# Kernel optimization log

Measured on AMD Instinct MI355X. Metric: run time of the kernel, lower is better.

## Reference

```python
import jax, jax.numpy as jnp
import numpy as np

B, S, D = 2, 1024, 768
E = 8
FF = 4 * D
TOP_K = 2
LN_EPS = 1e-5


def setup_inputs() -> dict:
    key = jax.random.key(0)
    ks = jax.random.split(key, 14)
    s = 0.02
    return {
        "x": jax.random.normal(ks[0], (B, S, D), dtype=jnp.float32),
        "router_w": jax.random.normal(ks[1], (D, E), dtype=jnp.float32) * s,
        "router_b": jnp.zeros((E,), dtype=jnp.float32),
        "dg_w": jax.random.normal(ks[2], (E, D), dtype=jnp.float32) * s,
        "dg_b": jnp.zeros((E,), dtype=jnp.float32),
        "w1_w": jax.random.normal(ks[3], (E, D, FF), dtype=jnp.float32) * s,
        "w1_b": jnp.zeros((E, FF), dtype=jnp.float32),
        "w2_w": jax.random.normal(ks[4], (E, FF, D), dtype=jnp.float32) * s,
        "w2_b": jnp.zeros((E, D), dtype=jnp.float32),
        "w3_w": jax.random.normal(ks[5], (E, D, FF), dtype=jnp.float32) * s,
        "w3_b": jnp.zeros((E, FF), dtype=jnp.float32),
        "ln_g": jnp.ones((E, D), dtype=jnp.float32),
        "ln_b": jnp.zeros((E, D), dtype=jnp.float32),
    }


def _moe_forward(x, router_w, router_b, dg_w, dg_b, w1_w, w1_b, w2_w, w2_b,
                 w3_w, w3_b, ln_g, ln_b):
    b, s, d = x.shape
    T = b * s
    xf = x.reshape(T, d)

    # Router (dropout is identity in eval mode)
    logits = xf @ router_w + router_b                      # [T, E]
    routing = jax.nn.softmax(logits, axis=-1)
    topk_w, topk_i = jax.lax.top_k(routing, TOP_K)          # [T, 2]
    topk_w = jax.nn.softmax(topk_w, axis=-1)                # renormalize via softmax (as in source)

    # Dense per-expert SwiGLU FFN over all tokens (faithful math, vectorized)
    h1 = jnp.einsum('td,edf->etf', xf, w1_w) + w1_b[:, None, :]   # [E, T, FF]
    gate = jax.nn.silu(jnp.einsum('td,edf->etf', xf, w3_w) + w3_b[:, None, :])
    ff = jnp.einsum('etf,efd->etd', jax.nn.silu(h1) * gate, w2_w) + w2_b[:, None, :]  # [E, T, D]
    dg = jax.nn.sigmoid(jnp.einsum('td,ed->et', xf, dg_w) + dg_b[:, None])            # [E, T]

    tok = jnp.arange(T)
    out = jnp.zeros_like(xf)
    for i in range(TOP_K):
        e = topk_i[:, i]                                    # [T]
        y = xf + dg[e, tok][:, None] * topk_w[:, i:i + 1] * ff[e, tok]  # [T, D]
        mu = jnp.mean(y, axis=-1, keepdims=True)
        var = jnp.mean(jnp.square(y - mu), axis=-1, keepdims=True)
        out = out + ((y - mu) / jnp.sqrt(var + LN_EPS)) * ln_g[e] + ln_b[e]

    expert_load = jnp.zeros((E,), dtype=jnp.float32).at[topk_i.reshape(-1)].add(1.0)
    return out.reshape(b, s, d), expert_load


def reference(x, router_w, router_b, dg_w, dg_b, w1_w, w1_b, w2_w, w2_b,
              w3_w, w3_b, ln_g, ln_b):
    return _moe_forward(x, router_w, router_b, dg_w, dg_b, w1_w, w1_b,
                        w2_w, w2_b, w3_w, w3_b, ln_g, ln_b)
```

## Files before the change

### kernel.cpp

```cpp
#include <hip/hip_runtime.h>
#include <math.h>

#define T 2048
#define D 768
#define E 8
#define FF 3072
#define NPOS (2 * T)
#define MAXTILE 40
#define PSTRIDE ((size_t)(NPOS + 128) * D)

using f32x4 = __attribute__((ext_vector_type(4))) float;

template<bool HI>
__device__ __forceinline__ unsigned f2fp8pk(float a, float b, unsigned old) {
    return __builtin_amdgcn_cvt_pk_fp8_f32(a, b, (int)old, HI);
}
__device__ __forceinline__ unsigned char f2fp8(float f) {
    return (unsigned char)(__builtin_amdgcn_cvt_pk_fp8_f32(f, 0.f, 0, false) & 0xff);
}
__device__ __forceinline__ float siluf(float v) {
    return v / (1.0f + __expf(-v));
}
__device__ __forceinline__ void gload16(const void* g, void* l) {
    __builtin_amdgcn_global_load_lds(
        (const __attribute__((address_space(1))) void*)g,
        (__attribute__((address_space(3))) void*)l, 16, 0, 0);
}

__device__ __forceinline__ void transpose128(const float* __restrict__ in,
                                             unsigned char* __restrict__ out,
                                             int C, int Rb, int r0, int c0,
                                             char* smem, int tid) {
    int wv = tid >> 6, lane = tid & 63;
    size_t rowB = (size_t)C * 4;
    const char* inb = (const char*)in + (size_t)r0 * rowB + (size_t)c0 * 4;
    const char* src_lane = inb + (size_t)(lane >> 5) * rowB + (lane & 31) * 16;
#pragma unroll
    for (int i = 0; i < 16; ++i) {
        int rpair = i * 4 + wv;
        gload16(src_lane + (size_t)(2 * rpair) * rowB, smem + rpair * 1024);
    }
    asm volatile("s_waitcnt vmcnt(0)" ::: "memory");
    __syncthreads();

    const float* fin = (const float*)smem;
    int cb = (tid & 31) * 4;
    int rgb = tid >> 5;
    unsigned pk[4][4];
#pragma unroll
    for (int p = 0; p < 4; ++p) {
        int rb = (rgb + 8 * p) * 4;
        float4 q0 = *(const float4*)(fin + (rb + 0) * 128 + cb);
        float4 q1 = *(const float4*)(fin + (rb + 1) * 128 + cb);
        float4 q2 = *(const float4*)(fin + (rb + 2) * 128 + cb);
        float4 q3 = *(const float4*)(fin + (rb + 3) * 128 + cb);
        unsigned w;
        w = f2fp8pk<false>(q0.x, q1.x, 0); w = f2fp8pk<true>(q2.x, q3.x, w); pk[p][0] = w;
        w = f2fp8pk<false>(q0.y, q1.y, 0); w = f2fp8pk<true>(q2.y, q3.y, w); pk[p][1] = w;
        w = f2fp8pk<false>(q0.z, q1.z, 0); w = f2fp8pk<true>(q2.z, q3.z, w); pk[p][2] = w;
        w = f2fp8pk<false>(q0.w, q1.w, 0); w = f2fp8pk<true>(q2.w, q3.w, w); pk[p][3] = w;
    }
    __syncthreads();
    unsigned* po = (unsigned*)smem;
#pragma unroll
    for (int p = 0; p < 4; ++p) {
        int rg = rgb + 8 * p;
#pragma unroll
        for (int j = 0; j < 4; ++j)
            po[(cb + j) * 33 + rg] = pk[p][j];
    }
    __syncthreads();
#pragma unroll
    for (int p = 0; p < 4; ++p) {
        int c = (tid >> 3) + 32 * p;
        int gs = tid & 7;
        const unsigned* bp = &po[c * 33 + gs * 4];
        uint4 val;
        val.x = bp[0]; val.y = bp[1]; val.z = bp[2]; val.w = bp[3];
        *(uint4*)(out + (size_t)(c0 + c) * Rb + r0 + gs * 16) = val;
    }
}

__global__ __launch_bounds__(256, 2)
void pre_kernel(const float* __restrict__ x,
                const float* __restrict__ rw, const float* __restrict__ rbias,
                const float* __restrict__ dgw, const float* __restrict__ dgb,
                const float* __restrict__ w1, const float* __restrict__ w3,
                unsigned char* __restrict__ xb,
                int* __restrict__ e_arr, float* __restrict__ s_arr,
                unsigned char* __restrict__ w1t, unsigned char* __restrict__ w3t) {
    __shared__ __align__(16) char smem[65536];
    int bid = blockIdx.x;
    int tid = threadIdx.x;

    if (bid >= 512) {
        int idx = bid - 512;
        int z = idx / 144;
        int rem = idx % 144;
        int r0 = (rem % 6) * 128;
        int c0 = (rem / 6) * 128;
        const float* in;
        unsigned char* outp;
        if (z < 8) { in = w1 + (size_t)z * D * FF; outp = w1t + (size_t)z * D * FF; }
        else       { in = w3 + (size_t)(z - 8) * D * FF; outp = w3t + (size_t)(z - 8) * D * FF; }
        transpose128(in, outp, FF, D, r0, c0, smem, tid);
        return;
    }

    int lane = tid & 63;
    int wv = tid >> 6;
    int t = bid * 4 + wv;

    float lg[E], dl[E];
#pragma unroll
    for (int e = 0; e < E; ++e) { lg[e] = 0.f; dl[e] = 0.f; }

    const float* xt = x + (size_t)t * D;
    unsigned char* xbt = xb + (size_t)t * D;
#pragma unroll
    for (int i = 0; i < D / 64; ++i) {
        int d = lane + 64 * i;
        float xv = xt[d];
        xbt[d] = f2fp8(xv);
#pragma unroll
        for (int e = 0; e < E; ++e) {
            lg[e] = fmaf(xv, rw[d * E + e], lg[e]);
            dl[e] = fmaf(xv, dgw[e * D + d], dl[e]);
        }
    }
#pragma unroll
    for (int e = 0; e < E; ++e) {
        for (int off = 32; off; off >>= 1) {
            lg[e] += __shfl_xor(lg[e], off);
            dl[e] += __shfl_xor(dl[e], off);
        }
    }
    if (lane == 0) {
        float p[E];
        float m = -1e30f;
#pragma unroll
        for (int e = 0; e < E; ++e) { lg[e] += rbias[e]; m = fmaxf(m, lg[e]); }
        float s = 0.f;
#pragma unroll
        for (int e = 0; e < E; ++e) { p[e] = __expf(lg[e] - m); s += p[e]; }
        float inv = 1.0f / s;
#pragma unroll
        for (int e = 0; e < E; ++e) p[e] *= inv;

        int i0 = 0; float b0 = p[0];
#pragma unroll
        for (int e = 1; e < E; ++e) if (p[e] > b0) { b0 = p[e]; i0 = e; }
        int i1 = -1; float b1 = -1.0f;
#pragma unroll
        for (int e = 0; e < E; ++e) if (e != i0 && p[e] > b1) { b1 = p[e]; i1 = e; }

        float eb = __expf(b1 - b0);
        float w0 = 1.0f / (1.0f + eb);
        float w1v = eb / (1.0f + eb);

        float dg0 = 1.0f / (1.0f + __expf(-(dl[i0] + dgb[i0])));
        float dg1 = 1.0f / (1.0f + __expf(-(dl[i1] + dgb[i1])));

        e_arr[t * 2 + 0] = i0;
        e_arr[t * 2 + 1] = i1;
        s_arr[t * 2 + 0] = dg0 * w0;
        s_arr[t * 2 + 1] = dg1 * w1v;
    }
}

__global__ __launch_bounds__(256)
void scan_assign_kernel(const int* __restrict__ e_arr,
                        float* __restrict__ load_out,
                        int* __restrict__ tme, int* __restrict__ tmm,
                        int* __restrict__ tml,
                        int* __restrict__ a_tok,
                        int* __restrict__ pos_of) {
    __shared__ int lcnt[E];
    __shared__ int lcur[E];
    int tid = threadIdx.x;
    if (tid < E) lcnt[tid] = 0;
    __syncthreads();
    for (int t = tid; t < T; t += 256) {
        atomicAdd(&lcnt[e_arr[t * 2]], 1);
        atomicAdd(&lcnt[e_arr[t * 2 + 1]], 1);
    }
    __syncthreads();
    if (tid == 0) {
        int b = 0, nt = 0;
        for (int e = 0; e < E; ++e) {
            int c = lcnt[e];
            lcur[e] = b;
            load_out[e] = (float)c;
            for (int m = 0; m < c; m += 128) {
                tme[nt] = e;
                tmm[nt] = b + m;
                tml[nt] = (c - m < 128) ? (c - m) : 128;
                ++nt;
            }
            b += c;
        }
        for (; nt < MAXTILE; ++nt) tme[nt] = -1;
    }
    __syncthreads();
    for (int t = tid; t < T; t += 256) {
#pragma unroll
        for (int s = 0; s < 2; ++s) {
            int e = e_arr[t * 2 + s];
            int pos = atomicAdd(&lcur[e], 1);
            a_tok[pos] = t;
            pos_of[t * 2 + s] = pos;
        }
    }
}

__global__ __launch_bounds__(256, 2)
void gemm1_w2t_kernel(const float* __restrict__ w2, unsigned char* __restrict__ w2t,
                      const unsigned char* __restrict__ xb,
                      const unsigned char* __restrict__ w1t, const float* __restrict__ w1b,
                      const unsigned char* __restrict__ w3t, const float* __restrict__ w3b,
                      const int* __restrict__ a_tok,
                      const int* __restrict__ tme, const int* __restrict__ tmm,
                      const int* __restrict__ tml,
                      unsigned char* __restrict__ acts) {
    __shared__ __align__(16) char smem[65536];
    int bid = blockIdx.x;
    int tid = threadIdx.x;

    if (bid < 1152) {
        int z = bid / 144;
        int rem = bid % 144;
        int r0 = (rem % 24) * 128;
        int c0 = (rem / 24) * 128;
        transpose128(w2 + (size_t)z * FF * D, w2t + (size_t)z * FF * D,
                     D, FF, r0, c0, smem, tid);
        return;
    }

    int g = bid - 1152;
    int mt = g / 48;
    int e = tme[mt];
    if (e < 0) return;
    int mstart = tmm[mt], mlen = tml[mt];
    int fBase = (g % 48) * 64;

    char (*As)[16384] = (char(*)[16384])smem;
    char (*Bs)[16384] = (char(*)[16384])(smem + 32768);

    int lane = tid & 63, wv = tid >> 6;
    int wr = wv & 1, wc = wv >> 1;
    int l15 = lane & 15, lk = lane >> 4;
    int lrow = lane >> 3;
    int swl = (((lane & 7) ^ lrow) << 4);

    const char* xbp = (const char*)xb;
    size_t aoff[4];
#pragma unroll
    for (int i = 0; i < 4; ++i) {
        int r = (wv + 4 * i) * 8 + lrow;
        int rr = r < mlen ? r : mlen - 1;
        aoff[i] = (size_t)a_tok[mstart + rr] * D + swl;
    }
    const char* w1p = (const char*)(w1t + (size_t)e * FF * D);
    const char* w3p = (const char*)(w3t + (size_t)e * FF * D);
    size_t boff[2];
#pragma unroll
    for (int i = 0; i < 2; ++i) {
        int f = (wv + 4 * i) * 8 + lrow;
        boff[i] = (size_t)(fBase + f) * D + swl;
    }

    auto stage = [&](int buf, int ks) {
        int kb = ks * 128;
        char* ab = &As[buf][0];
        char* bb = &Bs[buf][0];
#pragma unroll
        for (int i = 0; i < 4; ++i)
            gload16(xbp + aoff[i] + kb, ab + (wv + 4 * i) * 1024);
#pragma unroll
        for (int i = 0; i < 2; ++i) {
            gload16(w1p + boff[i] + kb, bb + (wv + 4 * i) * 1024);
            gload16(w3p + boff[i] + kb, bb + 8192 + (wv + 4 * i) * 1024);
        }
    };

    f32x4 hacc[4][2], gacc[4][2];
#pragma unroll
    for (int m = 0; m < 4; ++m)
#pragma unroll
        for (int n = 0; n < 2; ++n) {
            hacc[m][n] = f32x4{0.f, 0.f, 0.f, 0.f};
            gacc[m][n] = f32x4{0.f, 0.f, 0.f, 0.f};
        }

    stage(0, 0);
    stage(1, 1);
#pragma unroll 1
    for (int ks = 0; ks < 6; ++ks) {
        int cur = ks & 1;
        if (ks < 5) asm volatile("s_waitcnt vmcnt(8)" ::: "memory");
        else        asm volatile("s_waitcnt vmcnt(0)" ::: "memory");
        __builtin_amdgcn_s_barrier();
        const char* Ab = &As[cur][0];
        const char* Bb = &Bs[cur][0];
        __builtin_amdgcn_s_setprio(1);
#pragma unroll
        for (int ksub = 0; ksub < 4; ++ksub) {
            int koff = ksub * 32 + lk * 8;
            long af[4];
#pragma unroll
            for (int m = 0; m < 4; ++m) {
                int row = wr * 64 + m * 16 + l15;
                af[m] = *(const long*)(Ab + row * 128 + (koff ^ ((row & 7) << 4)));
            }
#pragma unroll
            for (int n = 0; n < 2; ++n) {
                int rowf = wc * 32 + n * 16 + l15;
                int off = rowf * 128 + (koff ^ ((rowf & 7) << 4));
                long b1 = *(const long*)(Bb + off);
                long b3 = *(const long*)(Bb + 8192 + off);
#pragma unroll
                for (int m = 0; m < 4; ++m) {
                    hacc[m][n] = __builtin_amdgcn_mfma_f32_16x16x32_fp8_fp8(af[m], b1, hacc[m][n], 0, 0, 0);
                    gacc[m][n] = __builtin_amdgcn_mfma_f32_16x16x32_fp8_fp8(af[m], b3, gacc[m][n], 0, 0, 0);
                }
            }
        }
        __builtin_amdgcn_s_setprio(0);
        __builtin_amdgcn_s_barrier();
        if (ks < 4) stage(cur, ks + 2);
    }

    unsigned char* al = (unsigned char*)&As[0][0];
    float b1v[2], b3v[2];
#pragma unroll
    for (int n = 0; n < 2; ++n) {
        int f = fBase + wc * 32 + n * 16 + l15;
        b1v[n] = w1b[e * FF + f];
        b3v[n] = w3b[e * FF + f];
    }
#pragma unroll
    for (int m = 0; m < 4; ++m)
#pragma unroll
        for (int n = 0; n < 2; ++n)
#pragma unroll
            for (int j = 0; j < 4; ++j) {
                float h = hacc[m][n][j] + b1v[n];
                float gg = gacc[m][n][j] + b3v[n];
                int row = wr * 64 + m * 16 + lk * 4 + j;
                int col = wc * 32 + n * 16 + l15;
                al[row * 64 + col] = f2fp8(siluf(h) * siluf(gg));
            }
    __syncthreads();
    int r = tid >> 1, cb = (tid & 1) * 32;
    if (r < mlen) {
        unsigned char* gp = acts + (size_t)(mstart + r) * FF + fBase + cb;
        const unsigned char* lp = al + r * 64 + cb;
        *(uint4*)(gp)      = *(const uint4*)(lp);
        *(uint4*)(gp + 16) = *(const uint4*)(lp + 16);
    }
}

__global__ __launch_bounds__(256, 2)
void gemm2_kernel(const unsigned char* __restrict__ acts,
                  const unsigned char* __restrict__ w2t,
                  const int* __restrict__ tme, const int* __restrict__ tmm,
                  const int* __restrict__ tml,
                  float* __restrict__ ffs) {
    int mt = blockIdx.y;
    int e = tme[mt];
    if (e < 0) return;
    int mstart = tmm[mt], mlen = tml[mt];
    int nBase = blockIdx.x * 128;
    int ksl = blockIdx.z;

    __shared__ char As[2][16384];
    __shared__ char Bs[2][16384];

    int tid = threadIdx.x;
    int lane = tid & 63, wv = tid >> 6;
    int wr = wv & 1, wc = wv >> 1;
    int l15 = lane & 15, lk = lane >> 4;
    int lrow = lane >> 3;
    int swl = (((lane & 7) ^ lrow) << 4);

    const char* ap = (const char*)acts;
    const char* w2p = (const char*)(w2t + (size_t)e * (size_t)D * FF);
    size_t aoff[4], boff[4];
#pragma unroll
    for (int i = 0; i < 4; ++i) {
        int r = (wv + 4 * i) * 8 + lrow;
        aoff[i] = (size_t)(mstart + r) * FF + swl;
        boff[i] = (size_t)(nBase + r) * FF + swl;
    }
    int kOff = ksl * (FF / 2);

    auto stage = [&](int buf, int ks) {
        int kb = kOff + ks * 128;
        char* ab = &As[buf][0];
        char* bb = &Bs[buf][0];
#pragma unroll
        for (int i = 0; i < 4; ++i) {
            gload16(ap + aoff[i] + kb, ab + (wv + 4 * i) * 1024);
            gload16(w2p + boff[i] + kb, bb + (wv + 4 * i) * 1024);
        }
    };

    f32x4 facc[4][4];
#pragma unroll
    for (int m = 0; m < 4; ++m)
#pragma unroll
        for (int n = 0; n < 4; ++n) facc[m][n] = f32x4{0.f, 0.f, 0.f, 0.f};

    stage(0, 0);
    stage(1, 1);
#pragma unroll 1
    for (int ks = 0; ks < 12; ++ks) {
        int cur = ks & 1;
        if (ks < 11) asm volatile("s_waitcnt vmcnt(8)" ::: "memory");
        else         asm volatile("s_waitcnt vmcnt(0)" ::: "memory");
        __builtin_amdgcn_s_barrier();
        const char* Ab = &As[cur][0];
        const char* Bb = &Bs[cur][0];
        __builtin_amdgcn_s_setprio(1);
#pragma unroll
        for (int ksub = 0; ksub < 4; ++ksub) {
            int koff = ksub * 32 + lk * 8;
            long af[4], bf[4];
#pragma unroll
            for (int m = 0; m < 4; ++m) {
                int row = wr * 64 + m * 16 + l15;
                af[m] = *(const long*)(Ab + row * 128 + (koff ^ ((row & 7) << 4)));
            }
#pragma unroll
            for (int n = 0; n < 4; ++n) {
                int row = wc * 64 + n * 16 + l15;
                bf[n] = *(const long*)(Bb + row * 128 + (koff ^ ((row & 7) << 4)));
            }
#pragma unroll
            for (int m = 0; m < 4; ++m)
#pragma unroll
                for (int n = 0; n < 4; ++n)
                    facc[m][n] = __builtin_amdgcn_mfma_f32_16x16x32_fp8_fp8(af[m], bf[n], facc[m][n], 0, 0, 0);
        }
        __builtin_amdgcn_s_setprio(0);
        __builtin_amdgcn_s_barrier();
        if (ks < 10) stage(cur, ks + 2);
    }

    float* op = ffs + (size_t)ksl * PSTRIDE;
#pragma unroll
    for (int m = 0; m < 4; ++m)
#pragma unroll
        for (int j = 0; j < 4; ++j) {
            int row = wr * 64 + m * 16 + lk * 4 + j;
            if (row < mlen) {
                float* gp = op + (size_t)(mstart + row) * D + nBase + wc * 64;
#pragma unroll
                for (int n = 0; n < 4; ++n)
                    gp[n * 16 + l15] = facc[m][n][j];
            }
        }
}

__global__ __launch_bounds__(256)
void combine_kernel(const float* __restrict__ x,
                    const float* __restrict__ ffs,
                    const int* __restrict__ e_arr,
                    const int* __restrict__ pos_of,
                    const float* __restrict__ s_arr,
                    const float* __restrict__ w2b,
                    const float* __restrict__ lng,
                    const float* __restrict__ lnb,
                    float* __restrict__ out) {
    int t = blockIdx.x;
    int tid = threadIdx.x;
    int p0 = pos_of[t * 2], p1 = pos_of[t * 2 + 1];
    int e0 = e_arr[t * 2], e1 = e_arr[t * 2 + 1];
    float sw0 = s_arr[t * 2], sw1 = s_arr[t * 2 + 1];
    __shared__ float red[4][4];

    float y0[3], y1[3];
    float s0 = 0.f, q0 = 0.f, s1 = 0.f, q1 = 0.f;
#pragma unroll
    for (int m = 0; m < 3; ++m) {
        int d = tid + 256 * m;
        float xv = x[(size_t)t * D + d];
        float f0 = ffs[(size_t)p0 * D + d] + ffs[PSTRIDE + (size_t)p0 * D + d] + w2b[e0 * D + d];
        float f1 = ffs[(size_t)p1 * D + d] + ffs[PSTRIDE + (size_t)p1 * D + d] + w2b[e1 * D + d];
        float a = xv + sw0 * f0;
        float bb = xv + sw1 * f1;
        y0[m] = a; y1[m] = bb;
        s0 += a; q0 += a * a;
        s1 += bb; q1 += bb * bb;
    }
    for (int off = 32; off; off >>= 1) {
        s0 += __shfl_xor(s0, off);
        q0 += __shfl_xor(q0, off);
        s1 += __shfl_xor(s1, off);
        q1 += __shfl_xor(q1, off);
    }
    int wv = tid >> 6, lane = tid & 63;
    if (lane == 0) { red[wv][0] = s0; red[wv][1] = q0; red[wv][2] = s1; red[wv][3] = q1; }
    __syncthreads();
    s0 = red[0][0] + red[1][0] + red[2][0] + red[3][0];
    q0 = red[0][1] + red[1][1] + red[2][1] + red[3][1];
    s1 = red[0][2] + red[1][2] + red[2][2] + red[3][2];
    q1 = red[0][3] + red[1][3] + red[2][3] + red[3][3];

    const float invD = 1.0f / (float)D;
    float mu0 = s0 * invD, var0 = q0 * invD - mu0 * mu0;
    float mu1 = s1 * invD, var1 = q1 * invD - mu1 * mu1;
    float r0 = rsqrtf(var0 + 1e-5f);
    float r1 = rsqrtf(var1 + 1e-5f);

#pragma unroll
    for (int m = 0; m < 3; ++m) {
        int d = tid + 256 * m;
        out[(size_t)t * D + d] =
            (y0[m] - mu0) * r0 * lng[e0 * D + d] + lnb[e0 * D + d] +
            (y1[m] - mu1) * r1 * lng[e1 * D + d] + lnb[e1 * D + d];
    }
}

extern "C" void kernel_launch(void* const* d_in, const int* in_sizes, int n_in,
                              void* d_out, int out_size, void* d_ws, size_t ws_size,
                              hipStream_t stream) {
    const float* x   = (const float*)d_in[0];
    const float* rw  = (const float*)d_in[1];
    const float* rb  = (const float*)d_in[2];
    const float* dgw = (const float*)d_in[3];
    const float* dgb = (const float*)d_in[4];
    const float* w1  = (const float*)d_in[5];
    const float* w1b = (const float*)d_in[6];
    const float* w2  = (const float*)d_in[7];
    const float* w2b = (const float*)d_in[8];
    const float* w3  = (const float*)d_in[9];
    const float* w3b = (const float*)d_in[10];
    const float* lng = (const float*)d_in[11];
    const float* lnb = (const float*)d_in[12];

    float* out = (float*)d_out;
    float* load_out = out + (size_t)T * D;

    char* w = (char*)d_ws;
    size_t off = 0;
    auto alloc = [&](size_t bytes) -> void* {
        void* p = w + off;
        off = (off + bytes + 255) & ~(size_t)255;
        return p;
    };
    int* e_arr    = (int*)alloc(NPOS * sizeof(int));
    int* a_tok    = (int*)alloc(NPOS * sizeof(int));
    int* pos_of   = (int*)alloc(NPOS * sizeof(int));
    float* s_arr  = (float*)alloc(NPOS * sizeof(float));
    int* tme      = (int*)alloc(MAXTILE * sizeof(int));
    int* tmm      = (int*)alloc(MAXTILE * sizeof(int));
    int* tml      = (int*)alloc(MAXTILE * sizeof(int));
    unsigned char* xb  = (unsigned char*)alloc((size_t)T * D);
    unsigned char* w1t = (unsigned char*)alloc((size_t)E * D * FF);
    unsigned char* w3t = (unsigned char*)alloc((size_t)E * D * FF);
    unsigned char* w2t = (unsigned char*)alloc((size_t)E * D * FF);
    unsigned char* acts = (unsigned char*)alloc((size_t)(NPOS + 128) * FF);
    float* ffs    = (float*)alloc(2 * PSTRIDE * sizeof(float));

    pre_kernel<<<512 + 2304, 256, 0, stream>>>(x, rw, rb, dgw, dgb, w1, w3,
                                               xb, e_arr, s_arr, w1t, w3t);
    scan_assign_kernel<<<1, 256, 0, stream>>>(e_arr, load_out, tme, tmm, tml,
                                              a_tok, pos_of);
    gemm1_w2t_kernel<<<1152 + 1920, 256, 0, stream>>>(
        w2, w2t, xb, w1t, w1b, w3t, w3b, a_tok, tme, tmm, tml, acts);
    gemm2_kernel<<<dim3(D / 128, MAXTILE, 2), 256, 0, stream>>>(
        acts, w2t, tme, tmm, tml, ffs);
    combine_kernel<<<T, 256, 0, stream>>>(x, ffs, e_arr, pos_of, s_arr, w2b, lng, lnb, out);
}
```

Before: 153.4 us.

## Process two M-tiles per gemm1 block with cross-tile prefetch pipelining

Measured after the change: 148.3 us. 3.3% less time.

```diff
diff --git a/kernel.cpp b/kernel.cpp
--- a/kernel.cpp
+++ b/kernel.cpp
@@ -222,13 +222,14 @@
                       const int* __restrict__ tme, const int* __restrict__ tmm,
                       const int* __restrict__ tml,
                       unsigned char* __restrict__ acts) {
-    __shared__ __align__(16) char smem[65536];
+    __shared__ __align__(16) char smem[73728];
     int bid = blockIdx.x;
     int tid = threadIdx.x;
 
-    if (bid < 1152) {
-        int z = bid / 144;
-        int rem = bid % 144;
+    if (bid >= 960) {
+        int idx = bid - 960;
+        int z = idx / 144;
+        int rem = idx % 144;
         int r0 = (rem % 24) * 128;
         int c0 = (rem / 24) * 128;
         transpose128(w2 + (size_t)z * FF * D, w2t + (size_t)z * FF * D,
@@ -236,15 +237,21 @@
         return;
     }
 
-    int g = bid - 1152;
-    int mt = g / 48;
-    int e = tme[mt];
-    if (e < 0) return;
-    int mstart = tmm[mt], mlen = tml[mt];
-    int fBase = (g % 48) * 64;
-
-    char (*As)[16384] = (char(*)[16384])smem;
-    char (*Bs)[16384] = (char(*)[16384])(smem + 32768);
+    int slot = bid / 48;
+    int fBase = (bid % 48) * 64;
+    int mt0 = slot * 2;
+    int e0 = tme[mt0];
+    if (e0 < 0) return;
+    int e1 = tme[mt0 + 1];
+    bool have2 = (e1 >= 0);
+    int mstart0 = tmm[mt0], mlen0 = tml[mt0];
+    int mstart1 = have2 ? tmm[mt0 + 1] : mstart0;
+    int mlen1   = have2 ? tml[mt0 + 1] : mlen0;
+    if (!have2) e1 = e0;
+
+    char* As = smem;
+    char* Bs = smem + 32768;
+    unsigned char* eplds = (unsigned char*)(smem + 65536);
 
     int lane = tid & 63, wv = tid >> 6;
     int wr = wv & 1, wc = wv >> 1;
@@ -253,15 +260,11 @@
     int swl = (((lane & 7) ^ lrow) << 4);
 
     const char* xbp = (const char*)xb;
-    size_t aoff[4];
-#pragma unroll
-    for (int i = 0; i < 4; ++i) {
-        int r = (wv + 4 * i) * 8 + lrow;
-        int rr = r < mlen ? r : mlen - 1;
-        aoff[i] = (size_t)a_tok[mstart + rr] * D + swl;
-    }
-    const char* w1p = (const char*)(w1t + (size_t)e * FF * D);
-    const char* w3p = (const char*)(w3t + (size_t)e * FF * D);
+    const char* w1p0 = (const char*)(w1t + (size_t)e0 * FF * D);
+    const char* w3p0 = (const char*)(w3t + (size_t)e0 * FF * D);
+    const char* w1p1 = (const char*)(w1t + (size_t)e1 * FF * D);
+    const char* w3p1 = (const char*)(w3t + (size_t)e1 * FF * D);
+
     size_t boff[2];
 #pragma unroll
     for (int i = 0; i < 2; ++i) {
@@ -269,39 +272,53 @@
         boff[i] = (size_t)(fBase + f) * D + swl;
     }
 
-    auto stage = [&](int buf, int ks) {
+    size_t a0[4], a1[4];
+#pragma unroll
+    for (int i = 0; i < 4; ++i) {
+        int r = (wv + 4 * i) * 8 + lrow;
+        int rr0 = r < mlen0 ? r : mlen0 - 1;
+        int rr1 = r < mlen1 ? r : mlen1 - 1;
+        a0[i] = (size_t)a_tok[mstart0 + rr0] * D + swl;
+        a1[i] = (size_t)a_tok[mstart1 + rr1] * D + swl;
+    }
+    float tb1[2][2], tb3[2][2];
+#pragma unroll
+    for (int n = 0; n < 2; ++n) {
+        int f = fBase + wc * 32 + n * 16 + l15;
+        tb1[0][n] = w1b[e0 * FF + f];
+        tb3[0][n] = w3b[e0 * FF + f];
+        tb1[1][n] = w1b[e1 * FF + f];
+        tb3[1][n] = w3b[e1 * FF + f];
+    }
+
+    auto stage = [&](int buf, const size_t* ao, const char* w1p_, const char* w3p_, int ks) {
         int kb = ks * 128;
-        char* ab = &As[buf][0];
-        char* bb = &Bs[buf][0];
+        char* ab = As + buf * 16384;
+        char* bb = Bs + buf * 16384;
 #pragma unroll
         for (int i = 0; i < 4; ++i)
-            gload16(xbp + aoff[i] + kb, ab + (wv + 4 * i) * 1024);
+            gload16(xbp + ao[i] + kb, ab + (wv + 4 * i) * 1024);
 #pragma unroll
         for (int i = 0; i < 2; ++i) {
-            gload16(w1p + boff[i] + kb, bb + (wv + 4 * i) * 1024);
-            gload16(w3p + boff[i] + kb, bb + 8192 + (wv + 4 * i) * 1024);
+            gload16(w1p_ + boff[i] + kb, bb + (wv + 4 * i) * 1024);
+            gload16(w3p_ + boff[i] + kb, bb + 8192 + (wv + 4 * i) * 1024);
         }
     };
 
     f32x4 hacc[4][2], gacc[4][2];
-#pragma unroll
-    for (int m = 0; m < 4; ++m)
-#pragma unroll
-        for (int n = 0; n < 2; ++n) {
-            hacc[m][n] = f32x4{0.f, 0.f, 0.f, 0.f};
-            gacc[m][n] = f32x4{0.f, 0.f, 0.f, 0.f};
-        }
-
-    stage(0, 0);
-    stage(1, 1);
-#pragma unroll 1
-    for (int ks = 0; ks < 6; ++ks) {
-        int cur = ks & 1;
-        if (ks < 5) asm volatile("s_waitcnt vmcnt(8)" ::: "memory");
-        else        asm volatile("s_waitcnt vmcnt(0)" ::: "memory");
-        __builtin_amdgcn_s_barrier();
-        const char* Ab = &As[cur][0];
-        const char* Bb = &Bs[cur][0];
+    auto zacc = [&]() {
+#pragma unroll
+        for (int m = 0; m < 4; ++m)
+#pragma unroll
+            for (int n = 0; n < 2; ++n) {
+                hacc[m][n] = f32x4{0.f, 0.f, 0.f, 0.f};
+                gacc[m][n] = f32x4{0.f, 0.f, 0.f, 0.f};
+            }
+    };
+
+    auto computeStep = [&](int buf) {
+        const char* Ab = As + buf * 16384;
+        const char* Bb = Bs + buf * 16384;
         __builtin_amdgcn_s_setprio(1);
 #pragma unroll
         for (int ksub = 0; ksub < 4; ++ksub) {
@@ -326,38 +343,63 @@
             }
         }
         __builtin_amdgcn_s_setprio(0);
-        __builtin_amdgcn_s_barrier();
-        if (ks < 4) stage(cur, ks + 2);
-    }
-
-    unsigned char* al = (unsigned char*)&As[0][0];
-    float b1v[2], b3v[2];
-#pragma unroll
-    for (int n = 0; n < 2; ++n) {
-        int f = fBase + wc * 32 + n * 16 + l15;
-        b1v[n] = w1b[e * FF + f];
-        b3v[n] = w3b[e * FF + f];
-    }
-#pragma unroll
-    for (int m = 0; m < 4; ++m)
-#pragma unroll
-        for (int n = 0; n < 2; ++n)
-#pragma unroll
-            for (int j = 0; j < 4; ++j) {
-                float h = hacc[m][n][j] + b1v[n];
-                float gg = gacc[m][n][j] + b3v[n];
-                int row = wr * 64 + m * 16 + lk * 4 + j;
-                int col = wc * 32 + n * 16 + l15;
-                al[row * 64 + col] = f2fp8(siluf(h) * siluf(gg));
-            }
-    __syncthreads();
-    int r = tid >> 1, cb = (tid & 1) * 32;
-    if (r < mlen) {
-        unsigned char* gp = acts + (size_t)(mstart + r) * FF + fBase + cb;
-        const unsigned char* lp = al + r * 64 + cb;
-        *(uint4*)(gp)      = *(const uint4*)(lp);
-        *(uint4*)(gp + 16) = *(const uint4*)(lp + 16);
-    }
+    };
+
+    auto epilogueT = [&](const float b1v[2], const float b3v[2], int mstart_, int mlen_) {
+#pragma unroll
+        for (int m = 0; m < 4; ++m)
+#pragma unroll
+            for (int n = 0; n < 2; ++n)
+#pragma unroll
+                for (int j = 0; j < 4; ++j) {
+                    float h = hacc[m][n][j] + b1v[n];
+                    float gg = gacc[m][n][j] + b3v[n];
+                    int row = wr * 64 + m * 16 + lk * 4 + j;
+                    int col = wc * 32 + n * 16 + l15;
+                    eplds[row * 64 + col] = f2fp8(siluf(h) * siluf(gg));
+                }
+        __syncthreads();
+        int r = tid >> 1, cb = (tid & 1) * 32;
+        if (r < mlen_) {
+            unsigned char* gp = acts + (size_t)(mstart_ + r) * FF + fBase + cb;
+            const unsigned char* lp = eplds + r * 64 + cb;
+            *(uint4*)(gp)      = *(const uint4*)(lp);
+            *(uint4*)(gp + 16) = *(const uint4*)(lp + 16);
+        }
+    };
+
+#define G1_WAIT8 asm volatile("s_waitcnt vmcnt(8)" ::: "memory")
+#define G1_BAR   __builtin_amdgcn_s_barrier()
+
+    zacc();
+    stage(0, a0, w1p0, w3p0, 0);
+    stage(1, a0, w1p0, w3p0, 1);
+    asm volatile("s_waitcnt vmcnt(0)" ::: "memory");
+    __syncthreads();
+
+     computeStep(0); G1_BAR; stage(0, a0, w1p0, w3p0, 2);
+     G1_BAR; computeStep(1); G1_BAR; stage(1, a0, w1p0, w3p0, 3);
+     G1_WAIT8; G1_BAR; computeStep(0); G1_BAR; stage(0, a0, w1p0, w3p0, 4);
+     G1_WAIT8; G1_BAR; computeStep(1); G1_BAR; stage(1, a0, w1p0, w3p0, 5);
+     G1_WAIT8; G1_BAR; computeStep(0); G1_BAR; stage(0, a1, w1p1, w3p1, 0);
+     G1_WAIT8; G1_BAR; computeStep(1); G1_BAR; stage(1, a1, w1p1, w3p1, 1);
+
+    epilogueT(tb1[0], tb3[0], mstart0, mlen0);
+    asm volatile("s_waitcnt vmcnt(0)" ::: "memory");
+    __syncthreads();
+
+    if (have2) {
+        zacc();
+         computeStep(0); G1_BAR; stage(0, a1, w1p1, w3p1, 2);
+         G1_BAR; computeStep(1); G1_BAR; stage(1, a1, w1p1, w3p1, 3);
+         G1_WAIT8; G1_BAR; computeStep(0); G1_BAR; stage(0, a1, w1p1, w3p1, 4);
+         G1_WAIT8; G1_BAR; computeStep(1); G1_BAR; stage(1, a1, w1p1, w3p1, 5);
+         G1_WAIT8; G1_BAR; computeStep(0); G1_BAR;
+         asm volatile("s_waitcnt vmcnt(0)" ::: "memory"); G1_BAR; computeStep(1); G1_BAR;
+        epilogueT(tb1[1], tb3[1], mstart1, mlen1);
+    }
+#undef G1_WAIT8
+#undef G1_BAR
 }
 
 __global__ __launch_bounds__(256, 2)
@@ -567,7 +609,7 @@
                                                xb, e_arr, s_arr, w1t, w3t);
     scan_assign_kernel<<<1, 256, 0, stream>>>(e_arr, load_out, tme, tmm, tml,
                                               a_tok, pos_of);
-    gemm1_w2t_kernel<<<1152 + 1920, 256, 0, stream>>>(
+    gemm1_w2t_kernel<<<960 + 1152, 256, 0, stream>>>(
         w2, w2t, xb, w1t, w1b, w3t, w3b, a_tok, tme, tmm, tml, acts);
     gemm2_kernel<<<dim3(D / 128, MAXTILE, 2), 256, 0, stream>>>(
         acts, w2t, tme, tmm, tml, ffs);
```
